# Kernel tuning notes

Hardware: AMD Instinct MI355X
Metric: run time of the kernel (lower is better)

The kernel has to match this reference:

```python
import jax, jax.numpy as jnp
import numpy as np

HEADS = 16
DIM_HEAD = 64
NUM_W = 4  # num_adaptive_weights
SCALE = DIM_HEAD ** -0.5


def setup_inputs() -> dict:
    key = jax.random.key(0)
    k0, k1, k2, k3 = jax.random.split(key, 4)
    b, n, dim = 2, 2048, 1024
    dim_inner = HEADS * DIM_HEAD  # 1024
    x = jax.random.normal(k0, (b, n, dim), jnp.float32)
    # Linear weights stored as (in, out); torch Linear(in,out,bias=False) computes x @ W.T
    Wqkv = jax.random.normal(k1, (dim, dim_inner * 3 * NUM_W), jnp.float32) * (dim ** -0.5)
    Wg = jax.random.normal(k2, (dim, NUM_W), jnp.float32) * (dim ** -0.5)
    Wout = jax.random.normal(k3, (dim_inner, dim * NUM_W), jnp.float32) * (dim_inner ** -0.5)
    mask = jnp.ones((b, n), dtype=bool)
    return {"x": x, "Wqkv": Wqkv, "Wg": Wg, "Wout": Wout, "mask": mask}


def reference(x, Wqkv, Wg, Wout, mask):
    b, n, dim = x.shape
    # to_qkv: packed last dim order is (qkv, h, d, w) per Rearrange 'b n (qkv h d w) -> qkv b h n d w'
    qkv = (x @ Wqkv).reshape(b, n, 3, HEADS, DIM_HEAD, NUM_W)
    qkv = jnp.transpose(qkv, (2, 0, 3, 1, 4, 5))  # [3, b, h, n, d, w]
    # adaptive gates: softmax over the w adaptive weights
    gates = jax.nn.softmax(x @ Wg, axis=-1)  # [b, n, w]
    # gated sum over adaptive-weight axis
    qkv = jnp.einsum('qbhndw,bnw->qbhnd', qkv, gates)
    q, k, v = qkv[0] * SCALE, qkv[1], qkv[2]
    sim = jnp.einsum('bhid,bhjd->bhij', q, k)  # [b, h, n, n]
    sim = jnp.where(mask[:, None, None, :], sim, jnp.finfo(sim.dtype).min)
    attn = jax.nn.softmax(sim, axis=-1)
    out = jnp.einsum('bhij,bhjd->bhid', attn, v)  # [b, h, n, d]
    out = out.transpose(0, 2, 1, 3).reshape(b, n, HEADS * DIM_HEAD)  # 'b h n d -> b n (h d)'
    out = (out @ Wout).reshape(b, n, dim, NUM_W)  # 'b n (d w) -> b n d w'
    # gated sum over w for the output projection
    return jnp.einsum('bndw,bnw->bnd', out, gates)
```

## Files before the change

### kernel.cpp

```cpp
#include <hip/hip_runtime.h>
#include <hip/hip_bf16.h>

#define M_TOT 4096
#define DIM_  1024
#define KP    4096
#define NC1   3072
#define NC2   1024

typedef unsigned short u16;
typedef unsigned int u32;
typedef unsigned long long u64;
typedef short bf16x8 __attribute__((ext_vector_type(8)));
typedef float f32x4 __attribute__((ext_vector_type(4)));

#define QSCALE 0.18033688011112042f
#define EXPOFF 20.0f

static __device__ __forceinline__ u16 f2bf(float f) {
    union { float f; u32 u; } v; v.f = f;
    u32 u = v.u;
    u += 0x7fffu + ((u >> 16) & 1u);
    return (u16)(u >> 16);
}
static __device__ __forceinline__ float bf2f(u16 h) {
    union { u32 u; float f; } v; v.u = ((u32)h) << 16; return v.f;
}

static __device__ __forceinline__ void gld_lds16(const u16* g, u16* l) {
    __builtin_amdgcn_global_load_lds(
        (__attribute__((address_space(1))) void*)(u64)g,
        (__attribute__((address_space(3))) void*)(u32)(u64)l,
        16, 0, 0);
}

#define SWZ_SCOL(lane) ((((lane) & 7) ^ (((lane) >> 3) & 7)) * 8)

__global__ __launch_bounds__(256) void gates_expand_kernel(const float* __restrict__ x,
                                                           const float* __restrict__ Wg,
                                                           float* __restrict__ gates,
                                                           u16* __restrict__ outA) {
    const int wid = threadIdx.x >> 6, lane = threadIdx.x & 63;
    const int m = blockIdx.x * 4 + wid;
    const float* xr = x + (size_t)m * DIM_;
    float a0 = 0.f, a1 = 0.f, a2 = 0.f, a3 = 0.f;
    for (int i = 0; i < DIM_ / 64; ++i) {
        int k = i * 64 + lane;
        float xv = xr[k];
        float4 wg = ((const float4*)Wg)[k];
        a0 += xv * wg.x; a1 += xv * wg.y; a2 += xv * wg.z; a3 += xv * wg.w;
    }
    for (int s = 1; s < 64; s <<= 1) {
        a0 += __shfl_xor(a0, s); a1 += __shfl_xor(a1, s);
        a2 += __shfl_xor(a2, s); a3 += __shfl_xor(a3, s);
    }
    float mx = fmaxf(fmaxf(a0, a1), fmaxf(a2, a3));
    float e0 = __expf(a0 - mx), e1 = __expf(a1 - mx), e2 = __expf(a2 - mx), e3 = __expf(a3 - mx);
    float inv = 1.0f / (e0 + e1 + e2 + e3);
    float g0 = e0 * inv, g1 = e1 * inv, g2 = e2 * inv, g3 = e3 * inv;
    if (lane == 0) ((float4*)gates)[m] = make_float4(g0, g1, g2, g3);
    ushort4* out4 = (ushort4*)outA;
    for (int i = 0; i < DIM_ / 64; ++i) {
        int k = i * 64 + lane;
        float val = xr[k];
        ushort4 o;
        o.x = f2bf(val * g0); o.y = f2bf(val * g1); o.z = f2bf(val * g2); o.w = f2bf(val * g3);
        out4[(size_t)m * 1024 + k] = o;
    }
}

__global__ __launch_bounds__(256) void expand_kernel(const u16* __restrict__ in,
                                                     const float* __restrict__ gates,
                                                     u16* __restrict__ outA) {
    size_t idx = (size_t)blockIdx.x * 256 + threadIdx.x;
    int m = (int)(idx >> 10);
    float val = bf2f(in[idx]);
    float4 g = ((const float4*)gates)[m];
    ushort4 o;
    o.x = f2bf(val * g.x); o.y = f2bf(val * g.y); o.z = f2bf(val * g.z); o.w = f2bf(val * g.w);
    ((ushort4*)outA)[idx] = o;
}

__global__ __launch_bounds__(256) void bprep_kernel(const float* __restrict__ src,
                                                    u16* __restrict__ dst,
                                                    int R, int Cg) {
    __shared__ u16 lds[64 * 68];
    const int t = threadIdx.x;
    const int cg0 = blockIdx.x * 16, k0 = blockIdx.y * 64;
    const float4* s4 = (const float4*)src;
    for (int i = 0; i < 4; ++i) {
        int f = i * 256 + t;
        int kl = f >> 4, f4 = f & 15;
        float4 v = s4[(size_t)(k0 + kl) * Cg + cg0 + f4];
        ushort4 o; o.x = f2bf(v.x); o.y = f2bf(v.y); o.z = f2bf(v.z); o.w = f2bf(v.w);
        *(ushort4*)&lds[kl * 68 + f4 * 4] = o;
    }
    __syncthreads();
    ushort4* d4 = (ushort4*)dst;
    for (int i = 0; i < 4; ++i) {
        int j = i * 256 + t;
        int cgl = j >> 6, kl = j & 63;
        d4[(size_t)(cg0 + cgl) * R + k0 + kl] = *(ushort4*)&lds[kl * 68 + cgl * 4];
    }
}

__global__ __launch_bounds__(256) void gemm1_kernel(const u16* __restrict__ A,
                                                    const u16* __restrict__ Bm,
                                                    u16* __restrict__ qbuf,
                                                    u16* __restrict__ kbuf,
                                                    u16* __restrict__ vbuf) {
    __shared__ u16 lA[128 * 64];
    __shared__ u16 lB[128 * 64];
    const int t = threadIdx.x;
    const int lane = t & 63, wid = t >> 6;
    const int wm = wid >> 1, wn = wid & 1;
    const int l15 = lane & 15, quad = lane >> 4;
    const int sx = l15 & 7;
    const int n0 = blockIdx.x * 128, m0 = blockIdx.y * 128;
    const int srow = lane >> 3, scol = SWZ_SCOL(lane);
    const u16* gA = A + (size_t)(m0 + wid * 32 + srow) * KP + scol;
    const u16* gB = Bm + (size_t)(n0 + wid * 32 + srow) * KP + scol;
    u16* lAw = &lA[wid * 2048];
    u16* lBw = &lB[wid * 2048];
    f32x4 acc[4][4] = {};
    for (int k0 = 0; k0 < KP; k0 += 64) {
        for (int i = 0; i < 4; ++i)
            gld_lds16(gA + (size_t)i * 8 * KP + k0, lAw + i * 512);
        for (int i = 0; i < 4; ++i)
            gld_lds16(gB + (size_t)i * 8 * KP + k0, lBw + i * 512);
        __syncthreads();
        for (int ks = 0; ks < 2; ++ks) {
            const int co = ((ks * 4 + quad) ^ sx) * 8;
            bf16x8 af[4], bfr[4];
            for (int mt = 0; mt < 4; ++mt)
                af[mt] = *(const bf16x8*)&lA[(wm * 64 + mt * 16 + l15) * 64 + co];
            for (int nt = 0; nt < 4; ++nt)
                bfr[nt] = *(const bf16x8*)&lB[(wn * 64 + nt * 16 + l15) * 64 + co];
            for (int mt = 0; mt < 4; ++mt)
                for (int nt = 0; nt < 4; ++nt)
                    acc[mt][nt] = __builtin_amdgcn_mfma_f32_16x16x32_bf16(af[mt], bfr[nt], acc[mt][nt], 0, 0, 0);
        }
        __syncthreads();
    }
    const int qkv = n0 >> 10;
    const int base_hd = n0 & 1023;
    for (int mt = 0; mt < 4; ++mt) {
        int mrow = m0 + wm * 64 + mt * 16 + quad * 4;
        int b = mrow >> 11, n = mrow & 2047;
        int bh0 = b * 16;
        for (int nt = 0; nt < 4; ++nt) {
            int hd = base_hd + wn * 64 + nt * 16 + l15;
            int h = hd >> 6, d = hd & 63;
            int bh = bh0 + h;
            if (qkv == 0) {
                for (int r = 0; r < 4; ++r)
                    qbuf[((size_t)bh * 2048 + n + r) * 64 + d] = f2bf(acc[mt][nt][r] * QSCALE);
            } else if (qkv == 1) {
                for (int r = 0; r < 4; ++r)
                    kbuf[((size_t)bh * 2048 + n + r) * 64 + d] = f2bf(acc[mt][nt][r]);
            } else {
                ushort4 o;
                o.x = f2bf(acc[mt][nt][0]); o.y = f2bf(acc[mt][nt][1]);
                o.z = f2bf(acc[mt][nt][2]); o.w = f2bf(acc[mt][nt][3]);
                *(ushort4*)&vbuf[((size_t)bh * 64 + d) * 2048 + n] = o;
            }
        }
    }
}

__global__ __launch_bounds__(256) void gemm2_kernel(const u16* __restrict__ A,
                                                    const u16* __restrict__ Bm,
                                                    float* __restrict__ outf) {
    __shared__ u16 lA[128 * 64];
    __shared__ u16 lB[64 * 64];
    const int t = threadIdx.x;
    const int lane = t & 63, wid = t >> 6;
    const int wm = wid >> 1, wn = wid & 1;
    const int l15 = lane & 15, quad = lane >> 4;
    const int sx = l15 & 7;
    const int n0 = blockIdx.x * 64, m0 = blockIdx.y * 128;
    const int srow = lane >> 3, scol = SWZ_SCOL(lane);
    const u16* gA = A + (size_t)(m0 + wid * 32 + srow) * KP + scol;
    const u16* gB = Bm + (size_t)(n0 + wid * 16 + srow) * KP + scol;
    u16* lAw = &lA[wid * 2048];
    u16* lBw = &lB[wid * 1024];
    f32x4 acc[4][2] = {};
    for (int k0 = 0; k0 < KP; k0 += 64) {
        for (int i = 0; i < 4; ++i)
            gld_lds16(gA + (size_t)i * 8 * KP + k0, lAw + i * 512);
        for (int i = 0; i < 2; ++i)
            gld_lds16(gB + (size_t)i * 8 * KP + k0, lBw + i * 512);
        __syncthreads();
        for (int ks = 0; ks < 2; ++ks) {
            const int co = ((ks * 4 + quad) ^ sx) * 8;
            bf16x8 af[4], bfr[2];
            for (int mt = 0; mt < 4; ++mt)
                af[mt] = *(const bf16x8*)&lA[(wm * 64 + mt * 16 + l15) * 64 + co];
            for (int nt = 0; nt < 2; ++nt)
                bfr[nt] = *(const bf16x8*)&lB[(wn * 32 + nt * 16 + l15) * 64 + co];
            for (int mt = 0; mt < 4; ++mt)
                for (int nt = 0; nt < 2; ++nt)
                    acc[mt][nt] = __builtin_amdgcn_mfma_f32_16x16x32_bf16(af[mt], bfr[nt], acc[mt][nt], 0, 0, 0);
        }
        __syncthreads();
    }
    for (int mt = 0; mt < 4; ++mt) {
        int mrow = m0 + wm * 64 + mt * 16 + quad * 4;
        for (int nt = 0; nt < 2; ++nt) {
            int col = n0 + wn * 32 + nt * 16 + l15;
            for (int r = 0; r < 4; ++r)
                outf[(size_t)(mrow + r) * NC2 + col] = acc[mt][nt][r];
        }
    }
}

__global__ __launch_bounds__(256) void attn_kernel(const u16* __restrict__ qbuf,
                                                   const u16* __restrict__ kbuf,
                                                   const u16* __restrict__ vbuf,
                                                   u16* __restrict__ outbuf) {
    __shared__ u16 lK[64 * 64];
    __shared__ u16 lV[64 * 64];
    __shared__ u16 lP[8 * 16 * 72];
    const int t = threadIdx.x, lane = t & 63, wq = t >> 6;
    const int l15 = lane & 15, quad = lane >> 4;
    const int sx = l15 & 7;
    const int bh = blockIdx.y, q0 = blockIdx.x * 128;
    const u16* Q = qbuf + (size_t)bh * 2048 * 64;
    const u16* K = kbuf + (size_t)bh * 2048 * 64;
    const u16* V = vbuf + (size_t)bh * 64 * 2048;
    bf16x8 qf[2][2];
    for (int mt = 0; mt < 2; ++mt)
        for (int ks = 0; ks < 2; ++ks)
            qf[mt][ks] = *(const bf16x8*)&Q[(size_t)(q0 + wq * 32 + mt * 16 + l15) * 64 + ks * 32 + quad * 8];
    f32x4 Oa[2][4] = {};
    float lacc[2] = {0.f, 0.f};
    const int srow = lane >> 3, scol = SWZ_SCOL(lane);
    const u16* gK = K + (size_t)(wq * 16 + srow) * 64 + scol;
    const u16* gV = V + (size_t)(wq * 16 + srow) * 2048 + scol;
    u16* lKw = &lK[wq * 16 * 64];
    u16* lVw = &lV[wq * 16 * 64];
    u16* lPw = &lP[wq * 2 * 16 * 72];
    for (int kt = 0; kt < 32; ++kt) {
        const int nk = kt * 64;
        __syncthreads();
        gld_lds16(gK + (size_t)nk * 64, lKw);
        gld_lds16(gK + (size_t)nk * 64 + 8 * 64, lKw + 512);
        gld_lds16(gV + nk, lVw);
        gld_lds16(gV + nk + 8 * 2048, lVw + 512);
        __syncthreads();
        f32x4 S[2][4] = {};
        for (int ks = 0; ks < 2; ++ks) {
            const int co = ((ks * 4 + quad) ^ sx) * 8;
            for (int nt = 0; nt < 4; ++nt) {
                bf16x8 kf = *(const bf16x8*)&lK[(nt * 16 + l15) * 64 + co];
                S[0][nt] = __builtin_amdgcn_mfma_f32_16x16x32_bf16(kf, qf[0][ks], S[0][nt], 0, 0, 0);
                S[1][nt] = __builtin_amdgcn_mfma_f32_16x16x32_bf16(kf, qf[1][ks], S[1][nt], 0, 0, 0);
            }
        }
        for (int mt = 0; mt < 2; ++mt) {
            u16* lPm = lPw + mt * (16 * 72);
            for (int nt = 0; nt < 4; ++nt) {
                float p0 = __builtin_amdgcn_exp2f(S[mt][nt][0] - EXPOFF);
                float p1 = __builtin_amdgcn_exp2f(S[mt][nt][1] - EXPOFF);
                float p2 = __builtin_amdgcn_exp2f(S[mt][nt][2] - EXPOFF);
                float p3 = __builtin_amdgcn_exp2f(S[mt][nt][3] - EXPOFF);
                lacc[mt] += (p0 + p1) + (p2 + p3);
                uint2 pk;
                pk.x = (u32)f2bf(p0) | ((u32)f2bf(p1) << 16);
                pk.y = (u32)f2bf(p2) | ((u32)f2bf(p3) << 16);
                *(uint2*)&lPm[l15 * 72 + nt * 16 + quad * 4] = pk;
            }
        }
        asm volatile("s_waitcnt lgkmcnt(0)" ::: "memory");
        for (int ks = 0; ks < 2; ++ks) {
            const int co = ((ks * 4 + quad) ^ sx) * 8;
            bf16x8 p0 = *(const bf16x8*)&lPw[0 * (16 * 72) + l15 * 72 + ks * 32 + quad * 8];
            bf16x8 p1 = *(const bf16x8*)&lPw[1 * (16 * 72) + l15 * 72 + ks * 32 + quad * 8];
            for (int dt = 0; dt < 4; ++dt) {
                bf16x8 vf = *(const bf16x8*)&lV[(dt * 16 + l15) * 64 + co];
                Oa[0][dt] = __builtin_amdgcn_mfma_f32_16x16x32_bf16(p0, vf, Oa[0][dt], 0, 0, 0);
                Oa[1][dt] = __builtin_amdgcn_mfma_f32_16x16x32_bf16(p1, vf, Oa[1][dt], 0, 0, 0);
            }
        }
    }
    for (int mt = 0; mt < 2; ++mt) {
        lacc[mt] += __shfl_xor(lacc[mt], 16);
        lacc[mt] += __shfl_xor(lacc[mt], 32);
    }
    const int b = bh >> 4, h = bh & 15;
    for (int mt = 0; mt < 2; ++mt) {
        for (int r = 0; r < 4; ++r) {
            int n = q0 + wq * 32 + mt * 16 + quad * 4 + r;
            float invl = 1.0f / __shfl(lacc[mt], quad * 4 + r);
            size_t rowbase = ((size_t)b * 2048 + n) * 1024 + h * 64;
            for (int dt = 0; dt < 4; ++dt)
                outbuf[rowbase + dt * 16 + l15] = f2bf(Oa[mt][dt][r] * invl);
        }
    }
}

extern "C" void kernel_launch(void* const* d_in, const int* in_sizes, int n_in,
                              void* d_out, int out_size, void* d_ws, size_t ws_size,
                              hipStream_t stream) {
    const float* x    = (const float*)d_in[0];
    const float* Wqkv = (const float*)d_in[1];
    const float* Wg   = (const float*)d_in[2];
    const float* Wout = (const float*)d_in[3];

    char* ws = (char*)d_ws;
    size_t off = 0;
    float* gates = (float*)(ws + off); off += (size_t)1 << 16;
    u16* Aexp = (u16*)(ws + off);      off += (size_t)M_TOT * KP * 2;
    char* regB = ws + off;             off += (size_t)NC1 * KP * 2;
    u16* B1 = (u16*)regB;
    u16* attn_out = (u16*)regB;
    u16* B2 = (u16*)(regB + (size_t)M_TOT * NC2 * 2);
    u16* qbuf = (u16*)(ws + off); off += (size_t)32 * 2048 * 64 * 2;
    u16* kbuf = (u16*)(ws + off); off += (size_t)32 * 2048 * 64 * 2;
    u16* vbuf = (u16*)(ws + off); off += (size_t)32 * 2048 * 64 * 2;

    hipLaunchKernelGGL(gates_expand_kernel, dim3(1024), dim3(256), 0, stream,
                       x, Wg, gates, Aexp);
    hipLaunchKernelGGL(bprep_kernel, dim3(192, 16), dim3(256), 0, stream,
                       Wqkv, B1, 1024, 3072);
    hipLaunchKernelGGL(gemm1_kernel, dim3(24, 32), dim3(256), 0, stream,
                       Aexp, B1, qbuf, kbuf, vbuf);
    hipLaunchKernelGGL(bprep_kernel, dim3(64, 16), dim3(256), 0, stream,
                       Wout, B2, 1024, 1024);
    hipLaunchKernelGGL(attn_kernel, dim3(16, 32), dim3(256), 0, stream,
                       qbuf, kbuf, vbuf, attn_out);
    hipLaunchKernelGGL(expand_kernel, dim3(16384), dim3(256), 0, stream,
                       attn_out, gates, Aexp);
    hipLaunchKernelGGL(gemm2_kernel, dim3(16, 32), dim3(256), 0, stream,
                       Aexp, B2, (float*)d_out);
}
```

Measured before the change: 395.5 us.

## Fuse gated expand into attention epilogue and widen K tiles to 128

The separate expand kernel is removed and its work moves into the attention epilogue. The epilogue now multiplies the normalized output by the four gates and writes the expanded bf16 A matrix for the output projection directly, which saves one intermediate write and read plus a launch. The attention kernel also processes 128 keys per iteration instead of 64, and gemm2 uses a K tile of 128 with a full 16-way XOR swizzle. Both changes halve the number of barrier-separated iterations at the cost of more LDS and more registers per block.

```diff
diff --git a/kernel.cpp b/kernel.cpp
--- a/kernel.cpp
+++ b/kernel.cpp
@@ -66,18 +66,6 @@
         o.x = f2bf(val * g0); o.y = f2bf(val * g1); o.z = f2bf(val * g2); o.w = f2bf(val * g3);
         out4[(size_t)m * 1024 + k] = o;
     }
-}
-
-__global__ __launch_bounds__(256) void expand_kernel(const u16* __restrict__ in,
-                                                     const float* __restrict__ gates,
-                                                     u16* __restrict__ outA) {
-    size_t idx = (size_t)blockIdx.x * 256 + threadIdx.x;
-    int m = (int)(idx >> 10);
-    float val = bf2f(in[idx]);
-    float4 g = ((const float4*)gates)[m];
-    ushort4 o;
-    o.x = f2bf(val * g.x); o.y = f2bf(val * g.y); o.z = f2bf(val * g.z); o.w = f2bf(val * g.w);
-    ((ushort4*)outA)[idx] = o;
 }
 
 __global__ __launch_bounds__(256) void bprep_kernel(const float* __restrict__ src,
@@ -170,33 +158,37 @@
 __global__ __launch_bounds__(256) void gemm2_kernel(const u16* __restrict__ A,
                                                     const u16* __restrict__ Bm,
                                                     float* __restrict__ outf) {
-    __shared__ u16 lA[128 * 64];
-    __shared__ u16 lB[64 * 64];
+    __shared__ u16 lA[128 * 128];
+    __shared__ u16 lB[64 * 128];
     const int t = threadIdx.x;
     const int lane = t & 63, wid = t >> 6;
     const int wm = wid >> 1, wn = wid & 1;
     const int l15 = lane & 15, quad = lane >> 4;
-    const int sx = l15 & 7;
     const int n0 = blockIdx.x * 64, m0 = blockIdx.y * 128;
-    const int srow = lane >> 3, scol = SWZ_SCOL(lane);
-    const u16* gA = A + (size_t)(m0 + wid * 32 + srow) * KP + scol;
-    const u16* gB = Bm + (size_t)(n0 + wid * 16 + srow) * KP + scol;
-    u16* lAw = &lA[wid * 2048];
-    u16* lBw = &lB[wid * 1024];
+    const int srow4 = lane >> 4;
+    const int schunk = lane & 15;
     f32x4 acc[4][2] = {};
-    for (int k0 = 0; k0 < KP; k0 += 64) {
-        for (int i = 0; i < 4; ++i)
-            gld_lds16(gA + (size_t)i * 8 * KP + k0, lAw + i * 512);
-        for (int i = 0; i < 2; ++i)
-            gld_lds16(gB + (size_t)i * 8 * KP + k0, lBw + i * 512);
-        __syncthreads();
-        for (int ks = 0; ks < 2; ++ks) {
-            const int co = ((ks * 4 + quad) ^ sx) * 8;
+    for (int k0 = 0; k0 < KP; k0 += 128) {
+        for (int i = 0; i < 8; ++i) {
+            int rr = i * 4 + srow4;
+            int sc = schunk ^ (rr & 15);
+            gld_lds16(A + (size_t)(m0 + wid * 32 + rr) * KP + k0 + sc * 8,
+                      &lA[(wid * 32 + i * 4) * 128]);
+        }
+        for (int i = 0; i < 4; ++i) {
+            int rr = i * 4 + srow4;
+            int sc = schunk ^ (rr & 15);
+            gld_lds16(Bm + (size_t)(n0 + wid * 16 + rr) * KP + k0 + sc * 8,
+                      &lB[(wid * 16 + i * 4) * 128]);
+        }
+        __syncthreads();
+        for (int ks = 0; ks < 4; ++ks) {
+            const int co = ((ks * 4 + quad) ^ l15) * 8;
             bf16x8 af[4], bfr[2];
             for (int mt = 0; mt < 4; ++mt)
-                af[mt] = *(const bf16x8*)&lA[(wm * 64 + mt * 16 + l15) * 64 + co];
+                af[mt] = *(const bf16x8*)&lA[(wm * 64 + mt * 16 + l15) * 128 + co];
             for (int nt = 0; nt < 2; ++nt)
-                bfr[nt] = *(const bf16x8*)&lB[(wn * 32 + nt * 16 + l15) * 64 + co];
+                bfr[nt] = *(const bf16x8*)&lB[(wn * 32 + nt * 16 + l15) * 128 + co];
             for (int mt = 0; mt < 4; ++mt)
                 for (int nt = 0; nt < 2; ++nt)
                     acc[mt][nt] = __builtin_amdgcn_mfma_f32_16x16x32_bf16(af[mt], bfr[nt], acc[mt][nt], 0, 0, 0);
@@ -216,13 +208,14 @@
 __global__ __launch_bounds__(256) void attn_kernel(const u16* __restrict__ qbuf,
                                                    const u16* __restrict__ kbuf,
                                                    const u16* __restrict__ vbuf,
-                                                   u16* __restrict__ outbuf) {
-    __shared__ u16 lK[64 * 64];
-    __shared__ u16 lV[64 * 64];
-    __shared__ u16 lP[8 * 16 * 72];
+                                                   const float* __restrict__ gates,
+                                                   u16* __restrict__ outA) {
+    __shared__ u16 lK[128 * 64];
+    __shared__ u16 lV[64 * 128];
+    __shared__ u16 lP[4 * 2 * 16 * 144];
     const int t = threadIdx.x, lane = t & 63, wq = t >> 6;
     const int l15 = lane & 15, quad = lane >> 4;
-    const int sx = l15 & 7;
+    const int sx7 = l15 & 7;
     const int bh = blockIdx.y, q0 = blockIdx.x * 128;
     const u16* Q = qbuf + (size_t)bh * 2048 * 64;
     const u16* K = kbuf + (size_t)bh * 2048 * 64;
@@ -233,32 +226,34 @@
             qf[mt][ks] = *(const bf16x8*)&Q[(size_t)(q0 + wq * 32 + mt * 16 + l15) * 64 + ks * 32 + quad * 8];
     f32x4 Oa[2][4] = {};
     float lacc[2] = {0.f, 0.f};
-    const int srow = lane >> 3, scol = SWZ_SCOL(lane);
-    const u16* gK = K + (size_t)(wq * 16 + srow) * 64 + scol;
-    const u16* gV = V + (size_t)(wq * 16 + srow) * 2048 + scol;
-    u16* lKw = &lK[wq * 16 * 64];
-    u16* lVw = &lV[wq * 16 * 64];
-    u16* lPw = &lP[wq * 2 * 16 * 72];
-    for (int kt = 0; kt < 32; ++kt) {
-        const int nk = kt * 64;
-        __syncthreads();
-        gld_lds16(gK + (size_t)nk * 64, lKw);
-        gld_lds16(gK + (size_t)nk * 64 + 8 * 64, lKw + 512);
-        gld_lds16(gV + nk, lVw);
-        gld_lds16(gV + nk + 8 * 2048, lVw + 512);
-        __syncthreads();
-        f32x4 S[2][4] = {};
+    const int krow = lane >> 3, kcol = SWZ_SCOL(lane);
+    const int vrow = lane >> 4, vchunk = lane & 15;
+    u16* lPw = &lP[wq * 2 * 16 * 144];
+    for (int kt = 0; kt < 16; ++kt) {
+        const int nk = kt * 128;
+        __syncthreads();
+        for (int i = 0; i < 4; ++i) {
+            int row = wq * 32 + i * 8 + krow;
+            gld_lds16(K + (size_t)(nk + row) * 64 + kcol, &lK[(wq * 32 + i * 8) * 64]);
+        }
+        for (int i = 0; i < 4; ++i) {
+            int row = wq * 16 + i * 4 + vrow;
+            int sc = vchunk ^ ((i * 4 + vrow) & 15);
+            gld_lds16(V + (size_t)row * 2048 + nk + sc * 8, &lV[(wq * 16 + i * 4) * 128]);
+        }
+        __syncthreads();
+        f32x4 S[2][8] = {};
         for (int ks = 0; ks < 2; ++ks) {
-            const int co = ((ks * 4 + quad) ^ sx) * 8;
-            for (int nt = 0; nt < 4; ++nt) {
+            const int co = ((ks * 4 + quad) ^ sx7) * 8;
+            for (int nt = 0; nt < 8; ++nt) {
                 bf16x8 kf = *(const bf16x8*)&lK[(nt * 16 + l15) * 64 + co];
                 S[0][nt] = __builtin_amdgcn_mfma_f32_16x16x32_bf16(kf, qf[0][ks], S[0][nt], 0, 0, 0);
                 S[1][nt] = __builtin_amdgcn_mfma_f32_16x16x32_bf16(kf, qf[1][ks], S[1][nt], 0, 0, 0);
             }
         }
         for (int mt = 0; mt < 2; ++mt) {
-            u16* lPm = lPw + mt * (16 * 72);
-            for (int nt = 0; nt < 4; ++nt) {
+            u16* lPm = lPw + mt * (16 * 144);
+            for (int nt = 0; nt < 8; ++nt) {
                 float p0 = __builtin_amdgcn_exp2f(S[mt][nt][0] - EXPOFF);
                 float p1 = __builtin_amdgcn_exp2f(S[mt][nt][1] - EXPOFF);
                 float p2 = __builtin_amdgcn_exp2f(S[mt][nt][2] - EXPOFF);
@@ -267,16 +262,16 @@
                 uint2 pk;
                 pk.x = (u32)f2bf(p0) | ((u32)f2bf(p1) << 16);
                 pk.y = (u32)f2bf(p2) | ((u32)f2bf(p3) << 16);
-                *(uint2*)&lPm[l15 * 72 + nt * 16 + quad * 4] = pk;
+                *(uint2*)&lPm[l15 * 144 + nt * 16 + quad * 4] = pk;
             }
         }
         asm volatile("s_waitcnt lgkmcnt(0)" ::: "memory");
-        for (int ks = 0; ks < 2; ++ks) {
-            const int co = ((ks * 4 + quad) ^ sx) * 8;
-            bf16x8 p0 = *(const bf16x8*)&lPw[0 * (16 * 72) + l15 * 72 + ks * 32 + quad * 8];
-            bf16x8 p1 = *(const bf16x8*)&lPw[1 * (16 * 72) + l15 * 72 + ks * 32 + quad * 8];
+        for (int ksp = 0; ksp < 4; ++ksp) {
+            const int cov = ((ksp * 4 + quad) ^ l15) * 8;
+            bf16x8 p0 = *(const bf16x8*)&lPw[0 * (16 * 144) + l15 * 144 + ksp * 32 + quad * 8];
+            bf16x8 p1 = *(const bf16x8*)&lPw[1 * (16 * 144) + l15 * 144 + ksp * 32 + quad * 8];
             for (int dt = 0; dt < 4; ++dt) {
-                bf16x8 vf = *(const bf16x8*)&lV[(dt * 16 + l15) * 64 + co];
+                bf16x8 vf = *(const bf16x8*)&lV[(dt * 16 + l15) * 128 + cov];
                 Oa[0][dt] = __builtin_amdgcn_mfma_f32_16x16x32_bf16(p0, vf, Oa[0][dt], 0, 0, 0);
                 Oa[1][dt] = __builtin_amdgcn_mfma_f32_16x16x32_bf16(p1, vf, Oa[1][dt], 0, 0, 0);
             }
@@ -287,13 +282,21 @@
         lacc[mt] += __shfl_xor(lacc[mt], 32);
     }
     const int b = bh >> 4, h = bh & 15;
+    ushort4* out4 = (ushort4*)outA;
+    const float4* gates4 = (const float4*)gates;
     for (int mt = 0; mt < 2; ++mt) {
         for (int r = 0; r < 4; ++r) {
             int n = q0 + wq * 32 + mt * 16 + quad * 4 + r;
+            int m = b * 2048 + n;
             float invl = 1.0f / __shfl(lacc[mt], quad * 4 + r);
-            size_t rowbase = ((size_t)b * 2048 + n) * 1024 + h * 64;
-            for (int dt = 0; dt < 4; ++dt)
-                outbuf[rowbase + dt * 16 + l15] = f2bf(Oa[mt][dt][r] * invl);
+            float4 g = gates4[m];
+            for (int dt = 0; dt < 4; ++dt) {
+                float val = Oa[mt][dt][r] * invl;
+                ushort4 o;
+                o.x = f2bf(val * g.x); o.y = f2bf(val * g.y);
+                o.z = f2bf(val * g.z); o.w = f2bf(val * g.w);
+                out4[(size_t)m * 1024 + h * 64 + dt * 16 + l15] = o;
+            }
         }
     }
 }
@@ -312,7 +315,6 @@
     u16* Aexp = (u16*)(ws + off);      off += (size_t)M_TOT * KP * 2;
     char* regB = ws + off;             off += (size_t)NC1 * KP * 2;
     u16* B1 = (u16*)regB;
-    u16* attn_out = (u16*)regB;
     u16* B2 = (u16*)(regB + (size_t)M_TOT * NC2 * 2);
     u16* qbuf = (u16*)(ws + off); off += (size_t)32 * 2048 * 64 * 2;
     u16* kbuf = (u16*)(ws + off); off += (size_t)32 * 2048 * 64 * 2;
@@ -327,9 +329,7 @@
     hipLaunchKernelGGL(bprep_kernel, dim3(64, 16), dim3(256), 0, stream,
                        Wout, B2, 1024, 1024);
     hipLaunchKernelGGL(attn_kernel, dim3(16, 32), dim3(256), 0, stream,
-                       qbuf, kbuf, vbuf, attn_out);
-    hipLaunchKernelGGL(expand_kernel, dim3(16384), dim3(256), 0, stream,
-                       attn_out, gates, Aexp);
+                       qbuf, kbuf, vbuf, gates, Aexp);
     hipLaunchKernelGGL(gemm2_kernel, dim3(16, 32), dim3(256), 0, stream,
                        Aexp, B2, (float*)d_out);
 }
```

Result: faster. 376.3 us (-4.9%).

## Double-buffer LDS in gemm2 and attention, fuse gate expansion into attention epilogue

Applied to the files above, without the earlier changes.

Gives gemm2 and the attention kernel ping-pong LDS buffers so the global-to-LDS load of the next K tile is issued right after the barrier and overlaps the MFMA work on the current tile. This replaces two __syncthreads per iteration with one raw barrier plus a vmcnt wait. It also folds the gate expansion into the attention epilogue, which writes gated bf16 rows straight into the gemm2 A buffer. That drops the separate expand kernel and its intermediate buffer round-trip. The cost is more LDS per block, which may lower occupancy, and an epilogue that now does four times the stores.

```diff
diff --git a/kernel.cpp b/kernel.cpp
--- a/kernel.cpp
+++ b/kernel.cpp
@@ -34,6 +34,10 @@
 }
 
 #define SWZ_SCOL(lane) ((((lane) & 7) ^ (((lane) >> 3) & 7)) * 8)
+
+#define RAW_BARRIER()   asm volatile("s_barrier" ::: "memory")
+#define WAIT_VM0()      asm volatile("s_waitcnt vmcnt(0)" ::: "memory")
+#define WAIT_LGKM0()    asm volatile("s_waitcnt lgkmcnt(0)" ::: "memory")
 
 __global__ __launch_bounds__(256) void gates_expand_kernel(const float* __restrict__ x,
                                                            const float* __restrict__ Wg,
@@ -66,18 +70,6 @@
         o.x = f2bf(val * g0); o.y = f2bf(val * g1); o.z = f2bf(val * g2); o.w = f2bf(val * g3);
         out4[(size_t)m * 1024 + k] = o;
     }
-}
-
-__global__ __launch_bounds__(256) void expand_kernel(const u16* __restrict__ in,
-                                                     const float* __restrict__ gates,
-                                                     u16* __restrict__ outA) {
-    size_t idx = (size_t)blockIdx.x * 256 + threadIdx.x;
-    int m = (int)(idx >> 10);
-    float val = bf2f(in[idx]);
-    float4 g = ((const float4*)gates)[m];
-    ushort4 o;
-    o.x = f2bf(val * g.x); o.y = f2bf(val * g.y); o.z = f2bf(val * g.z); o.w = f2bf(val * g.w);
-    ((ushort4*)outA)[idx] = o;
 }
 
 __global__ __launch_bounds__(256) void bprep_kernel(const float* __restrict__ src,
@@ -170,8 +162,8 @@
 __global__ __launch_bounds__(256) void gemm2_kernel(const u16* __restrict__ A,
                                                     const u16* __restrict__ Bm,
                                                     float* __restrict__ outf) {
-    __shared__ u16 lA[128 * 64];
-    __shared__ u16 lB[64 * 64];
+    __shared__ u16 lA[2][128 * 64];
+    __shared__ u16 lB[2][64 * 64];
     const int t = threadIdx.x;
     const int lane = t & 63, wid = t >> 6;
     const int wm = wid >> 1, wn = wid & 1;
@@ -181,27 +173,33 @@
     const int srow = lane >> 3, scol = SWZ_SCOL(lane);
     const u16* gA = A + (size_t)(m0 + wid * 32 + srow) * KP + scol;
     const u16* gB = Bm + (size_t)(n0 + wid * 16 + srow) * KP + scol;
-    u16* lAw = &lA[wid * 2048];
-    u16* lBw = &lB[wid * 1024];
+    for (int i = 0; i < 4; ++i)
+        gld_lds16(gA + (size_t)i * 8 * KP, &lA[0][(wid * 32 + i * 8) * 64]);
+    for (int i = 0; i < 2; ++i)
+        gld_lds16(gB + (size_t)i * 8 * KP, &lB[0][(wid * 16 + i * 8) * 64]);
     f32x4 acc[4][2] = {};
-    for (int k0 = 0; k0 < KP; k0 += 64) {
-        for (int i = 0; i < 4; ++i)
-            gld_lds16(gA + (size_t)i * 8 * KP + k0, lAw + i * 512);
-        for (int i = 0; i < 2; ++i)
-            gld_lds16(gB + (size_t)i * 8 * KP + k0, lBw + i * 512);
-        __syncthreads();
+    for (int it = 0; it < 64; ++it) {
+        const int cur = it & 1;
+        WAIT_VM0();
+        RAW_BARRIER();
+        if (it + 1 < 64) {
+            const int k0 = (it + 1) * 64, nb = cur ^ 1;
+            for (int i = 0; i < 4; ++i)
+                gld_lds16(gA + (size_t)i * 8 * KP + k0, &lA[nb][(wid * 32 + i * 8) * 64]);
+            for (int i = 0; i < 2; ++i)
+                gld_lds16(gB + (size_t)i * 8 * KP + k0, &lB[nb][(wid * 16 + i * 8) * 64]);
+        }
         for (int ks = 0; ks < 2; ++ks) {
             const int co = ((ks * 4 + quad) ^ sx) * 8;
             bf16x8 af[4], bfr[2];
             for (int mt = 0; mt < 4; ++mt)
-                af[mt] = *(const bf16x8*)&lA[(wm * 64 + mt * 16 + l15) * 64 + co];
+                af[mt] = *(const bf16x8*)&lA[cur][(wm * 64 + mt * 16 + l15) * 64 + co];
             for (int nt = 0; nt < 2; ++nt)
-                bfr[nt] = *(const bf16x8*)&lB[(wn * 32 + nt * 16 + l15) * 64 + co];
+                bfr[nt] = *(const bf16x8*)&lB[cur][(wn * 32 + nt * 16 + l15) * 64 + co];
             for (int mt = 0; mt < 4; ++mt)
                 for (int nt = 0; nt < 2; ++nt)
                     acc[mt][nt] = __builtin_amdgcn_mfma_f32_16x16x32_bf16(af[mt], bfr[nt], acc[mt][nt], 0, 0, 0);
         }
-        __syncthreads();
     }
     for (int mt = 0; mt < 4; ++mt) {
         int mrow = m0 + wm * 64 + mt * 16 + quad * 4;
@@ -216,13 +214,14 @@
 __global__ __launch_bounds__(256) void attn_kernel(const u16* __restrict__ qbuf,
                                                    const u16* __restrict__ kbuf,
                                                    const u16* __restrict__ vbuf,
-                                                   u16* __restrict__ outbuf) {
-    __shared__ u16 lK[64 * 64];
-    __shared__ u16 lV[64 * 64];
-    __shared__ u16 lP[8 * 16 * 72];
+                                                   const float* __restrict__ gates,
+                                                   u16* __restrict__ outA) {
+    __shared__ u16 lK[2][64 * 64];
+    __shared__ u16 lV[2][64 * 64];
+    __shared__ u16 lP[4][2 * 16 * 72];
     const int t = threadIdx.x, lane = t & 63, wq = t >> 6;
     const int l15 = lane & 15, quad = lane >> 4;
-    const int sx = l15 & 7;
+    const int sx7 = l15 & 7;
     const int bh = blockIdx.y, q0 = blockIdx.x * 128;
     const u16* Q = qbuf + (size_t)bh * 2048 * 64;
     const u16* K = kbuf + (size_t)bh * 2048 * 64;
@@ -233,25 +232,30 @@
             qf[mt][ks] = *(const bf16x8*)&Q[(size_t)(q0 + wq * 32 + mt * 16 + l15) * 64 + ks * 32 + quad * 8];
     f32x4 Oa[2][4] = {};
     float lacc[2] = {0.f, 0.f};
-    const int srow = lane >> 3, scol = SWZ_SCOL(lane);
-    const u16* gK = K + (size_t)(wq * 16 + srow) * 64 + scol;
-    const u16* gV = V + (size_t)(wq * 16 + srow) * 2048 + scol;
-    u16* lKw = &lK[wq * 16 * 64];
-    u16* lVw = &lV[wq * 16 * 64];
-    u16* lPw = &lP[wq * 2 * 16 * 72];
+    const int krow = lane >> 3, kcol = SWZ_SCOL(lane);
+    const u16* gK = K + (size_t)(wq * 16 + krow) * 64 + kcol;
+    const u16* gV = V + (size_t)(wq * 16 + krow) * 2048 + kcol;
+    u16* lPw = lP[wq];
+    gld_lds16(gK, &lK[0][(wq * 16) * 64]);
+    gld_lds16(gK + (size_t)8 * 64, &lK[0][(wq * 16 + 8) * 64]);
+    gld_lds16(gV, &lV[0][(wq * 16) * 64]);
+    gld_lds16(gV + (size_t)8 * 2048, &lV[0][(wq * 16 + 8) * 64]);
     for (int kt = 0; kt < 32; ++kt) {
-        const int nk = kt * 64;
-        __syncthreads();
-        gld_lds16(gK + (size_t)nk * 64, lKw);
-        gld_lds16(gK + (size_t)nk * 64 + 8 * 64, lKw + 512);
-        gld_lds16(gV + nk, lVw);
-        gld_lds16(gV + nk + 8 * 2048, lVw + 512);
-        __syncthreads();
+        const int cur = kt & 1;
+        WAIT_VM0();
+        RAW_BARRIER();
+        if (kt + 1 < 32) {
+            const int nxt = (kt + 1) * 64, nb = cur ^ 1;
+            gld_lds16(gK + (size_t)nxt * 64, &lK[nb][(wq * 16) * 64]);
+            gld_lds16(gK + (size_t)(nxt + 8) * 64, &lK[nb][(wq * 16 + 8) * 64]);
+            gld_lds16(gV + nxt, &lV[nb][(wq * 16) * 64]);
+            gld_lds16(gV + nxt + (size_t)8 * 2048, &lV[nb][(wq * 16 + 8) * 64]);
+        }
         f32x4 S[2][4] = {};
         for (int ks = 0; ks < 2; ++ks) {
-            const int co = ((ks * 4 + quad) ^ sx) * 8;
+            const int co = ((ks * 4 + quad) ^ sx7) * 8;
             for (int nt = 0; nt < 4; ++nt) {
-                bf16x8 kf = *(const bf16x8*)&lK[(nt * 16 + l15) * 64 + co];
+                bf16x8 kf = *(const bf16x8*)&lK[cur][(nt * 16 + l15) * 64 + co];
                 S[0][nt] = __builtin_amdgcn_mfma_f32_16x16x32_bf16(kf, qf[0][ks], S[0][nt], 0, 0, 0);
                 S[1][nt] = __builtin_amdgcn_mfma_f32_16x16x32_bf16(kf, qf[1][ks], S[1][nt], 0, 0, 0);
             }
@@ -270,13 +274,13 @@
                 *(uint2*)&lPm[l15 * 72 + nt * 16 + quad * 4] = pk;
             }
         }
-        asm volatile("s_waitcnt lgkmcnt(0)" ::: "memory");
+        WAIT_LGKM0();
         for (int ks = 0; ks < 2; ++ks) {
-            const int co = ((ks * 4 + quad) ^ sx) * 8;
+            const int co = ((ks * 4 + quad) ^ sx7) * 8;
             bf16x8 p0 = *(const bf16x8*)&lPw[0 * (16 * 72) + l15 * 72 + ks * 32 + quad * 8];
             bf16x8 p1 = *(const bf16x8*)&lPw[1 * (16 * 72) + l15 * 72 + ks * 32 + quad * 8];
             for (int dt = 0; dt < 4; ++dt) {
-                bf16x8 vf = *(const bf16x8*)&lV[(dt * 16 + l15) * 64 + co];
+                bf16x8 vf = *(const bf16x8*)&lV[cur][(dt * 16 + l15) * 64 + co];
                 Oa[0][dt] = __builtin_amdgcn_mfma_f32_16x16x32_bf16(p0, vf, Oa[0][dt], 0, 0, 0);
                 Oa[1][dt] = __builtin_amdgcn_mfma_f32_16x16x32_bf16(p1, vf, Oa[1][dt], 0, 0, 0);
             }
@@ -287,13 +291,21 @@
         lacc[mt] += __shfl_xor(lacc[mt], 32);
     }
     const int b = bh >> 4, h = bh & 15;
+    ushort4* out4 = (ushort4*)outA;
+    const float4* gates4 = (const float4*)gates;
     for (int mt = 0; mt < 2; ++mt) {
         for (int r = 0; r < 4; ++r) {
             int n = q0 + wq * 32 + mt * 16 + quad * 4 + r;
+            int m = b * 2048 + n;
             float invl = 1.0f / __shfl(lacc[mt], quad * 4 + r);
-            size_t rowbase = ((size_t)b * 2048 + n) * 1024 + h * 64;
-            for (int dt = 0; dt < 4; ++dt)
-                outbuf[rowbase + dt * 16 + l15] = f2bf(Oa[mt][dt][r] * invl);
+            float4 g = gates4[m];
+            for (int dt = 0; dt < 4; ++dt) {
+                float val = Oa[mt][dt][r] * invl;
+                ushort4 o;
+                o.x = f2bf(val * g.x); o.y = f2bf(val * g.y);
+                o.z = f2bf(val * g.z); o.w = f2bf(val * g.w);
+                out4[(size_t)m * 1024 + h * 64 + dt * 16 + l15] = o;
+            }
         }
     }
 }
@@ -312,7 +324,6 @@
     u16* Aexp = (u16*)(ws + off);      off += (size_t)M_TOT * KP * 2;
     char* regB = ws + off;             off += (size_t)NC1 * KP * 2;
     u16* B1 = (u16*)regB;
-    u16* attn_out = (u16*)regB;
     u16* B2 = (u16*)(regB + (size_t)M_TOT * NC2 * 2);
     u16* qbuf = (u16*)(ws + off); off += (size_t)32 * 2048 * 64 * 2;
     u16* kbuf = (u16*)(ws + off); off += (size_t)32 * 2048 * 64 * 2;
@@ -327,9 +338,7 @@
     hipLaunchKernelGGL(bprep_kernel, dim3(64, 16), dim3(256), 0, stream,
                        Wout, B2, 1024, 1024);
     hipLaunchKernelGGL(attn_kernel, dim3(16, 32), dim3(256), 0, stream,
-                       qbuf, kbuf, vbuf, attn_out);
-    hipLaunchKernelGGL(expand_kernel, dim3(16384), dim3(256), 0, stream,
-                       attn_out, gates, Aexp);
+                       qbuf, kbuf, vbuf, gates, Aexp);
     hipLaunchKernelGGL(gemm2_kernel, dim3(16, 32), dim3(256), 0, stream,
                        Aexp, B2, (float*)d_out);
 }
```

Measured after the change: 360.5 us. 8.8% less time.
